# Performance work log

Hardware: AMD Instinct MI355X
Metric: run time of the kernel (lower is better)

## Reference

```python
import jax, jax.numpy as jnp
import numpy as np

B, L, D, H = 64, 1024, 64, 512
LN_EPS = 1e-5


def setup_inputs() -> dict:
    key = jax.random.key(0)
    ks = jax.random.split(key, 10)
    s = 1.0 / np.sqrt(H)  # torch GRU/Linear default uniform init bound
    u = lambda k, shape: jax.random.uniform(k, shape, jnp.float32, -s, s)
    return {
        "x": jax.random.normal(ks[0], (B, L, D), jnp.float32),
        "h0": jnp.zeros((1, B, H), jnp.float32),
        "W_ih": u(ks[1], (3 * H, D)),   # gate order: r, z, n
        "W_hh": u(ks[2], (3 * H, H)),
        "b_ih": u(ks[3], (3 * H,)),
        "b_hh": u(ks[4], (3 * H,)),
        "gamma": jnp.ones((H,), jnp.float32),
        "beta": jnp.zeros((H,), jnp.float32),
        "W_pred": u(ks[5], (D, H)),
        "b_pred": u(ks[6], (D,)),
    }


def _gru_forward(x, h0, W_ih, W_hh, b_ih, b_hh):
    # Precompute input projections for all timesteps in one big GEMM.
    gi = jnp.einsum('bld,gd->blg', x, W_ih) + b_ih          # (B, L, 3H)
    gi = jnp.moveaxis(gi, 1, 0)                              # (L, B, 3H)

    def step(h, gi_t):
        gh = h @ W_hh.T + b_hh                               # (B, 3H)
        i_r, i_z, i_n = jnp.split(gi_t, 3, axis=-1)
        h_r, h_z, h_n = jnp.split(gh, 3, axis=-1)
        r = jax.nn.sigmoid(i_r + h_r)
        z = jax.nn.sigmoid(i_z + h_z)
        n = jnp.tanh(i_n + r * h_n)
        h_new = (1.0 - z) * n + z * h                        # PyTorch GRU update
        return h_new, h_new

    hN, hs = jax.lax.scan(step, h0[0], gi)                   # hs: (L, B, H)
    return jnp.moveaxis(hs, 0, 1), hN[None]                  # (B, L, H), (1, B, H)


def reference(x, h0, W_ih, W_hh, b_ih, b_hh, gamma, beta, W_pred, b_pred):
    h_raw, hN = _gru_forward(x, h0, W_ih, W_hh, b_ih, b_hh)
    mu = h_raw.mean(-1, keepdims=True)
    var = ((h_raw - mu) ** 2).mean(-1, keepdims=True)
    h_seq = (h_raw - mu) * jax.lax.rsqrt(var + LN_EPS) * gamma + beta
    x_hat = h_seq @ W_pred.T + b_pred                        # (B, L, D)
    return h_seq, hN, x_hat
```

## Files before the change

### kernel.cpp

```cpp
#include <hip/hip_runtime.h>

typedef unsigned short ushort_t;
typedef unsigned int uint32;
typedef unsigned long long uint64;
typedef __attribute__((ext_vector_type(8))) __bf16 bf16x8;
typedef __attribute__((ext_vector_type(4))) float f32x4;

#define BB 64
#define LL 1024
#define DD 64
#define HH 512
#define HSEQ_N (BB * LL * HH)
#define HN_OFF HSEQ_N
#define XH_OFF (HSEQ_N + BB * HH)

#define NGRP 4
#define NBLK 8
#define NT 4
#define WS_HEX_OFF 1024
#define WS_PS_OFF (1024 + 2 * NGRP * 16 * 512 * 2)

__device__ __forceinline__ ushort_t f2bf(float f) {
  union { float f; uint32 i; } v; v.f = f;
  uint32 r = (v.i + 0x7fffu + ((v.i >> 16) & 1u)) >> 16;
  return (ushort_t)r;
}
__device__ __forceinline__ __bf16 u2b(ushort_t u) {
  union { ushort_t u; __bf16 b; } v; v.u = u; return v.b;
}
__device__ __forceinline__ bf16x8 cvt8(const float* p) {
  float4 a = *(const float4*)p;
  float4 b = *(const float4*)(p + 4);
  bf16x8 r;
  r[0] = u2b(f2bf(a.x)); r[1] = u2b(f2bf(a.y)); r[2] = u2b(f2bf(a.z)); r[3] = u2b(f2bf(a.w));
  r[4] = u2b(f2bf(b.x)); r[5] = u2b(f2bf(b.y)); r[6] = u2b(f2bf(b.z)); r[7] = u2b(f2bf(b.w));
  return r;
}
__device__ __forceinline__ float sigm(float x) { return 1.0f / (1.0f + __expf(-x)); }
__device__ __forceinline__ float tanh_f(float x) {
  x = fminf(20.f, fmaxf(-20.f, x));
  float e = __expf(2.0f * x);
  return (e - 1.0f) / (e + 1.0f);
}

__device__ __forceinline__ void st_u32_agent(uint32* p, uint32 v) {
  __hip_atomic_store(p, v, __ATOMIC_RELAXED, __HIP_MEMORY_SCOPE_AGENT);
}
__device__ __forceinline__ void st_u64_agent(uint64* p, uint64 v) {
  __hip_atomic_store(p, v, __ATOMIC_RELAXED, __HIP_MEMORY_SCOPE_AGENT);
}
__device__ __forceinline__ uint64 ld_u64_agent(const uint64* p) {
  return __hip_atomic_load((uint64*)p, __ATOMIC_RELAXED, __HIP_MEMORY_SCOPE_AGENT);
}

__global__ __launch_bounds__(768) void gru_kernel(
    const float* __restrict__ x, const float* __restrict__ h0,
    const float* __restrict__ Wih, const float* __restrict__ Whh,
    const float* __restrict__ bih, const float* __restrict__ bhh,
    const float* __restrict__ gamma, const float* __restrict__ beta,
    float* __restrict__ out, uint32* __restrict__ cnt,
    ushort_t* __restrict__ h_ex, float2* __restrict__ ps_ex)
{
  __shared__ __align__(16) ushort_t Abuf[16 * 520];
  __shared__ __align__(16) ushort_t xbuf[16 * 80];
  __shared__ float grz[8][16 * 17];
  __shared__ float2 statb[16];

  const int tid = threadIdx.x;
  const int v = tid >> 6, lane = tid & 63, lo = lane & 15, hi = lane >> 4;
  const int s = v >> 2, T = v & 3;
  const int g = blockIdx.x & 3, c = blockIdx.x >> 2;
  const int b0 = g * 16;
  const int colj = c * 64 + T * 16 + lo;
  const int rowW = s * HH + colj;

  bf16x8 wB[16], wI[2];
  {
    const float* wr = Whh + (size_t)rowW * HH + hi * 8;
    #pragma unroll
    for (int ks = 0; ks < 16; ++ks) wB[ks] = cvt8(wr + ks * 32);
    const float* wir = Wih + (size_t)rowW * DD + hi * 8;
    #pragma unroll
    for (int ks = 0; ks < 2; ++ks) wI[ks] = cvt8(wir + ks * 32);
  }
  const float bsum = bih[rowW] + bhh[rowW];
  const float bgh = bhh[rowW];
  const float bgi = bih[rowW];

  float hprev[4], gmv = 0.f, btv = 0.f;
  if (s == 2) {
    gmv = gamma[colj]; btv = beta[colj];
    #pragma unroll
    for (int i = 0; i < 4; ++i) hprev[i] = h0[(size_t)(b0 + hi * 4 + i) * HH + colj];
  }

  for (int i = tid; i < 16 * 512; i += 768) {
    int row = i >> 9, col = i & 511;
    Abuf[row * 520 + col] = f2bf(h0[(size_t)(b0 + row) * HH + col]);
  }
  for (int i = tid; i < 1024; i += 768) {
    int row = i >> 6, d = i & 63;
    xbuf[row * 80 + d] = f2bf(x[((size_t)(b0 + row) * LL + 0) * DD + d]);
  }
  __syncthreads();

  uint32* fb = cnt + g * 64;

  for (int t = 0; t < LL; ++t) {
    float xr[2];
    if (v > 0) {
      int t1 = (t + 1 < LL) ? (t + 1) : (LL - 1);
      int n = 0;
      for (int i = tid - 64; i < 1024; i += 704, ++n)
        xr[n] = x[((size_t)(b0 + (i >> 6)) * LL + t1) * DD + (i & 63)];
    }

    f32x4 a0, a1, agi;
    #pragma unroll
    for (int i = 0; i < 4; ++i) {
      a0[i] = (s < 2) ? bsum : bgh;
      a1[i] = 0.f;
      agi[i] = bgi;
    }
    #pragma unroll
    for (int ks = 0; ks < 2; ++ks) {
      bf16x8 av = *(const bf16x8*)&xbuf[lo * 80 + ks * 32 + hi * 8];
      if (s < 2) a0 = __builtin_amdgcn_mfma_f32_16x16x32_bf16(av, wI[ks], a0, 0, 0, 0);
      else       agi = __builtin_amdgcn_mfma_f32_16x16x32_bf16(av, wI[ks], agi, 0, 0, 0);
    }
    #pragma unroll
    for (int ks = 0; ks < 16; ++ks) {
      bf16x8 av = *(const bf16x8*)&Abuf[lo * 520 + ks * 32 + hi * 8];
      if (ks & 1) a1 = __builtin_amdgcn_mfma_f32_16x16x32_bf16(av, wB[ks], a1, 0, 0, 0);
      else        a0 = __builtin_amdgcn_mfma_f32_16x16x32_bf16(av, wB[ks], a0, 0, 0, 0);
    }
    f32x4 gacc;
    #pragma unroll
    for (int i = 0; i < 4; ++i) gacc[i] = a0[i] + a1[i];

    if (s < 2) {
      #pragma unroll
      for (int i = 0; i < 4; ++i) grz[s * 4 + T][(hi * 4 + i) * 17 + lo] = sigm(gacc[i]);
    }
    __syncthreads();

    if (s == 2) {
      float hn[4];
      #pragma unroll
      for (int i = 0; i < 4; ++i) {
        float r = grz[T][(hi * 4 + i) * 17 + lo];
        float z = grz[4 + T][(hi * 4 + i) * 17 + lo];
        float n = tanh_f(agi[i] + r * gacc[i]);
        hn[i] = z * (hprev[i] - n) + n;
      }
      uint32* hx32 = (uint32*)(h_ex + (size_t)(((t & 1) * NGRP + g) * 16) * 512);
      {
        uint32 pk[4];
        #pragma unroll
        for (int i = 0; i < 4; ++i) {
          uint32 m = (uint32)f2bf(hn[i]);
          uint32 o = (uint32)__shfl_xor((int)m, 1, 64);
          pk[i] = (lo & 1) ? ((o & 0xffffu) | (m << 16)) : (m | (o << 16));
        }
        int p = lo & 1;
        int cb = c * 32 + T * 8 + (lo >> 1);
        st_u32_agent(&hx32[(hi * 4 + 2 * p) * 256 + cb], pk[2 * p]);
        st_u32_agent(&hx32[(hi * 4 + 2 * p + 1) * 256 + cb], pk[2 * p + 1]);
      }
      #pragma unroll
      for (int i = 0; i < 4; ++i) {
        float sv = hn[i], sq = hn[i] * hn[i];
        #pragma unroll
        for (int m = 1; m < 16; m <<= 1) {
          sv += __shfl_xor(sv, m, 64);
          sq += __shfl_xor(sq, m, 64);
        }
        if (lo == 0) {
          float2* pp = ps_ex + ((size_t)((t & 1) * NGRP + g) * 32 + (c * 4 + T)) * 16;
          union { float2 f; uint64 u; } uu; uu.f = make_float2(sv, sq);
          st_u64_agent((uint64*)&pp[hi * 4 + i], uu.u);
        }
      }
      if (t == LL - 1) {
        #pragma unroll
        for (int i = 0; i < 4; ++i)
          out[(size_t)HN_OFF + (size_t)(b0 + hi * 4 + i) * HH + colj] = hn[i];
      }
      #pragma unroll
      for (int i = 0; i < 4; ++i) hprev[i] = hn[i];
    }
    __syncthreads();

    if (tid == 0) st_u32_agent(&fb[c * 8], (uint32)(t + 1));
    if (v > 0) {
      int n = 0;
      for (int i = tid - 64; i < 1024; i += 704, ++n)
        xbuf[(i >> 6) * 80 + (i & 63)] = f2bf(xr[n]);
    }
    if (v == 0) {
      const uint32 tgt = (uint32)(t + 1);
      while (true) {
        uint32 f = (lane < 8)
          ? __hip_atomic_load(&fb[lane * 8], __ATOMIC_RELAXED, __HIP_MEMORY_SCOPE_AGENT)
          : tgt;
        if (__all((int)(f >= tgt))) break;
        __builtin_amdgcn_s_sleep(1);
      }
    }
    __syncthreads();

    if (v != 3) {
      const uint64* hx8 = (const uint64*)(h_ex + (size_t)(((t & 1) * NGRP + g) * 16) * 512);
      int sid = (v < 3) ? tid : tid - 64;
      for (int i = sid; i < 2048; i += 704) {
        uint64 vv = ld_u64_agent(hx8 + i);
        int row = i >> 7, c8 = i & 127;
        *(uint64*)&Abuf[row * 520 + c8 * 4] = vv;
      }
    } else {
      int r = lane >> 2, q = lane & 3;
      const float2* pp = ps_ex + (size_t)((t & 1) * NGRP + g) * 32 * 16;
      float sv = 0.f, sq = 0.f;
      #pragma unroll
      for (int j = 0; j < 8; ++j) {
        int u = q * 8 + j;
        union { uint64 u64; float2 f; } uu;
        uu.u64 = ld_u64_agent((const uint64*)&pp[u * 16 + r]);
        sv += uu.f.x; sq += uu.f.y;
      }
      sv += __shfl_xor(sv, 1, 64); sq += __shfl_xor(sq, 1, 64);
      sv += __shfl_xor(sv, 2, 64); sq += __shfl_xor(sq, 2, 64);
      if (q == 0) {
        float mu = sv * (1.0f / 512.0f);
        float var = sq * (1.0f / 512.0f) - mu * mu;
        statb[r] = make_float2(mu, rsqrtf(var + 1e-5f));
      }
    }
    __syncthreads();

    if (s == 2) {
      #pragma unroll
      for (int i = 0; i < 4; ++i) {
        float2 st = statb[hi * 4 + i];
        float y = (hprev[i] - st.x) * st.y * gmv + btv;
        out[((size_t)(b0 + hi * 4 + i) * LL + t) * HH + colj] = y;
      }
    }
  }
}

__global__ __launch_bounds__(256) void pred_kernel(
    float* __restrict__ out, const float* __restrict__ Wp, const float* __restrict__ bp)
{
  const int tid = threadIdx.x;
  const int v = tid >> 6, lane = tid & 63, lo = lane & 15, hi = lane >> 4;
  const int d = v * 16 + lo;

  bf16x8 wP[16];
  const float* wr = Wp + (size_t)d * HH + hi * 8;
  #pragma unroll
  for (int ks = 0; ks < 16; ++ks) wP[ks] = cvt8(wr + ks * 32);
  const float bpf = bp[d];

  #pragma unroll
  for (int rt = 0; rt < 2; ++rt) {
    const size_t row0 = ((size_t)blockIdx.x * 2 + rt) * 16;
    const float* ap = out + (row0 + lo) * HH + hi * 8;
    f32x4 acc;
    #pragma unroll
    for (int i = 0; i < 4; ++i) acc[i] = 0.f;
    #pragma unroll
    for (int ks = 0; ks < 16; ++ks) {
      bf16x8 av = cvt8(ap + ks * 32);
      acc = __builtin_amdgcn_mfma_f32_16x16x32_bf16(av, wP[ks], acc, 0, 0, 0);
    }
    #pragma unroll
    for (int i = 0; i < 4; ++i)
      out[(size_t)XH_OFF + (row0 + hi * 4 + i) * DD + d] = acc[i] + bpf;
  }
}

extern "C" void kernel_launch(void* const* d_in, const int* in_sizes, int n_in,
                              void* d_out, int out_size, void* d_ws, size_t ws_size,
                              hipStream_t stream) {
  const float* x   = (const float*)d_in[0];
  const float* h0  = (const float*)d_in[1];
  const float* Wih = (const float*)d_in[2];
  const float* Whh = (const float*)d_in[3];
  const float* bih = (const float*)d_in[4];
  const float* bhh = (const float*)d_in[5];
  const float* gam = (const float*)d_in[6];
  const float* bet = (const float*)d_in[7];
  const float* Wp  = (const float*)d_in[8];
  const float* bp  = (const float*)d_in[9];
  float* out = (float*)d_out;

  uint32* cnt    = (uint32*)d_ws;
  ushort_t* h_ex = (ushort_t*)((char*)d_ws + WS_HEX_OFF);
  float2* ps_ex  = (float2*)((char*)d_ws + WS_PS_OFF);

  hipMemsetAsync(d_ws, 0, 1024, stream);

  hipLaunchKernelGGL(gru_kernel, dim3(NGRP * NBLK), dim3(768), 0, stream,
                     x, h0, Wih, Whh, bih, bhh, gam, bet, out, cnt, h_ex, ps_ex);
  hipLaunchKernelGGL(pred_kernel, dim3(BB * LL / 32), dim3(256), 0, stream,
                     out, Wp, bp);
}
```

Before: 4.836 ms.

## Replace flag barrier with per-word tagged exchange polling in GRU recurrence

The per-step cross-block synchronization (counter flags plus a polling wave and two block barriers) is replaced by tagging every exchanged hidden-state word and LayerNorm partial sum with the timestep. Readers spin directly on the data until every tag matches. This removes the flag round trip and one __syncthreads per step. The r/z waves now poll and fill Abuf while the n-gate waves compute, and x prefetch and the stats reduction move onto the n-gate waves. The cost is doubled exchange traffic, since each 32-bit payload now travels with a 32-bit tag, plus a larger workspace memset.

```diff
diff --git a/kernel.cpp b/kernel.cpp
--- a/kernel.cpp
+++ b/kernel.cpp
@@ -16,9 +16,9 @@
 
 #define NGRP 4
 #define NBLK 8
-#define NT 4
 #define WS_HEX_OFF 1024
-#define WS_PS_OFF (1024 + 2 * NGRP * 16 * 512 * 2)
+#define WS_PS_OFF (1024 + 2 * NGRP * 16 * 256 * 8)
+#define WS_TOTAL (WS_PS_OFF + 2 * NGRP * 32 * 16 * 2 * 8)
 
 __device__ __forceinline__ ushort_t f2bf(float f) {
   union { float f; uint32 i; } v; v.f = f;
@@ -43,9 +43,6 @@
   return (e - 1.0f) / (e + 1.0f);
 }
 
-__device__ __forceinline__ void st_u32_agent(uint32* p, uint32 v) {
-  __hip_atomic_store(p, v, __ATOMIC_RELAXED, __HIP_MEMORY_SCOPE_AGENT);
-}
 __device__ __forceinline__ void st_u64_agent(uint64* p, uint64 v) {
   __hip_atomic_store(p, v, __ATOMIC_RELAXED, __HIP_MEMORY_SCOPE_AGENT);
 }
@@ -58,8 +55,7 @@
     const float* __restrict__ Wih, const float* __restrict__ Whh,
     const float* __restrict__ bih, const float* __restrict__ bhh,
     const float* __restrict__ gamma, const float* __restrict__ beta,
-    float* __restrict__ out, uint32* __restrict__ cnt,
-    ushort_t* __restrict__ h_ex, float2* __restrict__ ps_ex)
+    float* __restrict__ out, uint64* __restrict__ h_ex, uint64* __restrict__ ps_ex)
 {
   __shared__ __align__(16) ushort_t Abuf[16 * 520];
   __shared__ __align__(16) ushort_t xbuf[16 * 80];
@@ -104,15 +100,16 @@
   }
   __syncthreads();
 
-  uint32* fb = cnt + g * 64;
-
   for (int t = 0; t < LL; ++t) {
-    float xr[2];
-    if (v > 0) {
+    float xr[6];
+    if (v >= 9) {
       int t1 = (t + 1 < LL) ? (t + 1) : (LL - 1);
-      int n = 0;
-      for (int i = tid - 64; i < 1024; i += 704, ++n)
-        xr[n] = x[((size_t)(b0 + (i >> 6)) * LL + t1) * DD + (i & 63)];
+      int sid = tid - 576;
+      #pragma unroll
+      for (int k = 0; k < 6; ++k) {
+        int i = sid + k * 192;
+        if (i < 1024) xr[k] = x[((size_t)(b0 + (i >> 6)) * LL + t1) * DD + (i & 63)];
+      }
     }
 
     f32x4 a0, a1, agi;
@@ -144,7 +141,29 @@
     }
     __syncthreads();
 
-    if (s == 2) {
+    const uint32 tag = (uint32)(t + 1);
+    uint64* hx = h_ex + (size_t)((t & 1) * NGRP + g) * 4096;
+
+    if (s < 2) {
+      uint64 vals[8];
+      #pragma unroll
+      for (int k = 0; k < 8; ++k) vals[k] = ld_u64_agent(hx + tid + k * 512);
+      while (true) {
+        int bad = 0;
+        #pragma unroll
+        for (int k = 0; k < 8; ++k) bad |= ((uint32)vals[k] != tag);
+        if (!bad) break;
+        #pragma unroll
+        for (int k = 0; k < 8; ++k)
+          if ((uint32)vals[k] != tag) vals[k] = ld_u64_agent(hx + tid + k * 512);
+      }
+      #pragma unroll
+      for (int k = 0; k < 8; ++k) {
+        int idx = tid + k * 512;
+        int row = idx >> 8, cb = idx & 255;
+        *(uint32*)&Abuf[row * 520 + cb * 2] = (uint32)(vals[k] >> 32);
+      }
+    } else {
       float hn[4];
       #pragma unroll
       for (int i = 0; i < 4; ++i) {
@@ -153,7 +172,6 @@
         float n = tanh_f(agi[i] + r * gacc[i]);
         hn[i] = z * (hprev[i] - n) + n;
       }
-      uint32* hx32 = (uint32*)(h_ex + (size_t)(((t & 1) * NGRP + g) * 16) * 512);
       {
         uint32 pk[4];
         #pragma unroll
@@ -164,9 +182,11 @@
         }
         int p = lo & 1;
         int cb = c * 32 + T * 8 + (lo >> 1);
-        st_u32_agent(&hx32[(hi * 4 + 2 * p) * 256 + cb], pk[2 * p]);
-        st_u32_agent(&hx32[(hi * 4 + 2 * p + 1) * 256 + cb], pk[2 * p + 1]);
-      }
+        int r0 = hi * 4 + 2 * p;
+        st_u64_agent(&hx[r0 * 256 + cb], ((uint64)pk[2 * p] << 32) | tag);
+        st_u64_agent(&hx[(r0 + 1) * 256 + cb], ((uint64)pk[2 * p + 1] << 32) | tag);
+      }
+      uint64* pu = ps_ex + (size_t)((t & 1) * NGRP + g) * 1024;
       #pragma unroll
       for (int i = 0; i < 4; ++i) {
         float sv = hn[i], sq = hn[i] * hn[i];
@@ -176,9 +196,10 @@
           sq += __shfl_xor(sq, m, 64);
         }
         if (lo == 0) {
-          float2* pp = ps_ex + ((size_t)((t & 1) * NGRP + g) * 32 + (c * 4 + T)) * 16;
-          union { float2 f; uint64 u; } uu; uu.f = make_float2(sv, sq);
-          st_u64_agent((uint64*)&pp[hi * 4 + i], uu.u);
+          union { float f; uint32 u; } fv, fq; fv.f = sv; fq.f = sq;
+          int e = ((c * 4 + T) * 16 + (hi * 4 + i)) * 2;
+          st_u64_agent(&pu[e], ((uint64)fv.u << 32) | tag);
+          st_u64_agent(&pu[e + 1], ((uint64)fq.u << 32) | tag);
         }
       }
       if (t == LL - 1) {
@@ -188,52 +209,54 @@
       }
       #pragma unroll
       for (int i = 0; i < 4; ++i) hprev[i] = hn[i];
-    }
-    __syncthreads();
-
-    if (tid == 0) st_u32_agent(&fb[c * 8], (uint32)(t + 1));
-    if (v > 0) {
-      int n = 0;
-      for (int i = tid - 64; i < 1024; i += 704, ++n)
-        xbuf[(i >> 6) * 80 + (i & 63)] = f2bf(xr[n]);
-    }
-    if (v == 0) {
-      const uint32 tgt = (uint32)(t + 1);
-      while (true) {
-        uint32 f = (lane < 8)
-          ? __hip_atomic_load(&fb[lane * 8], __ATOMIC_RELAXED, __HIP_MEMORY_SCOPE_AGENT)
-          : tgt;
-        if (__all((int)(f >= tgt))) break;
-        __builtin_amdgcn_s_sleep(1);
-      }
-    }
-    __syncthreads();
-
-    if (v != 3) {
-      const uint64* hx8 = (const uint64*)(h_ex + (size_t)(((t & 1) * NGRP + g) * 16) * 512);
-      int sid = (v < 3) ? tid : tid - 64;
-      for (int i = sid; i < 2048; i += 704) {
-        uint64 vv = ld_u64_agent(hx8 + i);
-        int row = i >> 7, c8 = i & 127;
-        *(uint64*)&Abuf[row * 520 + c8 * 4] = vv;
-      }
-    } else {
-      int r = lane >> 2, q = lane & 3;
-      const float2* pp = ps_ex + (size_t)((t & 1) * NGRP + g) * 32 * 16;
-      float sv = 0.f, sq = 0.f;
-      #pragma unroll
-      for (int j = 0; j < 8; ++j) {
-        int u = q * 8 + j;
-        union { uint64 u64; float2 f; } uu;
-        uu.u64 = ld_u64_agent((const uint64*)&pp[u * 16 + r]);
-        sv += uu.f.x; sq += uu.f.y;
-      }
-      sv += __shfl_xor(sv, 1, 64); sq += __shfl_xor(sq, 1, 64);
-      sv += __shfl_xor(sv, 2, 64); sq += __shfl_xor(sq, 2, 64);
-      if (q == 0) {
-        float mu = sv * (1.0f / 512.0f);
-        float var = sq * (1.0f / 512.0f) - mu * mu;
-        statb[r] = make_float2(mu, rsqrtf(var + 1e-5f));
+
+      if (v >= 9) {
+        int sid = tid - 576;
+        #pragma unroll
+        for (int k = 0; k < 6; ++k) {
+          int i = sid + k * 192;
+          if (i < 1024) xbuf[(i >> 6) * 80 + (i & 63)] = f2bf(xr[k]);
+        }
+      }
+      if (v == 8) {
+        int r = lane >> 2, q = lane & 3;
+        const uint64* pb = ps_ex + (size_t)((t & 1) * NGRP + g) * 1024;
+        uint64 va[8], vb[8];
+        #pragma unroll
+        for (int j = 0; j < 8; ++j) {
+          int u = q * 8 + j;
+          int e = (u * 16 + r) * 2;
+          va[j] = ld_u64_agent(pb + e);
+          vb[j] = ld_u64_agent(pb + e + 1);
+        }
+        while (true) {
+          int bad = 0;
+          #pragma unroll
+          for (int j = 0; j < 8; ++j)
+            bad |= ((uint32)va[j] != tag) | ((uint32)vb[j] != tag);
+          if (!bad) break;
+          #pragma unroll
+          for (int j = 0; j < 8; ++j) {
+            int u = q * 8 + j;
+            int e = (u * 16 + r) * 2;
+            if ((uint32)va[j] != tag) va[j] = ld_u64_agent(pb + e);
+            if ((uint32)vb[j] != tag) vb[j] = ld_u64_agent(pb + e + 1);
+          }
+        }
+        float sv = 0.f, sq = 0.f;
+        #pragma unroll
+        for (int j = 0; j < 8; ++j) {
+          union { uint32 u; float f; } ua, ub;
+          ua.u = (uint32)(va[j] >> 32); ub.u = (uint32)(vb[j] >> 32);
+          sv += ua.f; sq += ub.f;
+        }
+        sv += __shfl_xor(sv, 1, 64); sq += __shfl_xor(sq, 1, 64);
+        sv += __shfl_xor(sv, 2, 64); sq += __shfl_xor(sq, 2, 64);
+        if (q == 0) {
+          float mu = sv * (1.0f / 512.0f);
+          float var = sq * (1.0f / 512.0f) - mu * mu;
+          statb[r] = make_float2(mu, rsqrtf(var + 1e-5f));
+        }
       }
     }
     __syncthreads();
@@ -295,14 +318,13 @@
   const float* bp  = (const float*)d_in[9];
   float* out = (float*)d_out;
 
-  uint32* cnt    = (uint32*)d_ws;
-  ushort_t* h_ex = (ushort_t*)((char*)d_ws + WS_HEX_OFF);
-  float2* ps_ex  = (float2*)((char*)d_ws + WS_PS_OFF);
-
-  hipMemsetAsync(d_ws, 0, 1024, stream);
+  uint64* h_ex = (uint64*)((char*)d_ws + WS_HEX_OFF);
+  uint64* ps_ex = (uint64*)((char*)d_ws + WS_PS_OFF);
+
+  hipMemsetAsync(d_ws, 0, WS_TOTAL, stream);
 
   hipLaunchKernelGGL(gru_kernel, dim3(NGRP * NBLK), dim3(768), 0, stream,
-                     x, h0, Wih, Whh, bih, bhh, gam, bet, out, cnt, h_ex, ps_ex);
+                     x, h0, Wih, Whh, bih, bhh, gam, bet, out, h_ex, ps_ex);
   hipLaunchKernelGGL(pred_kernel, dim3(BB * LL / 32), dim3(256), 0, stream,
                      out, Wp, bp);
 }
```

New measurement: 6.575 ms. +35.9%, slower.

## Use per-wave flags and 4-deep exchange buffers to remove per-step block barriers

Applied to the files above, without the earlier changes.

Each n-gate wave now publishes its own readiness flag after draining its global stores, instead of one thread per block signalling after a block-wide barrier. Non-n waves spin on all 32 flags and pull the exchanged hidden state directly. One n-gate wave computes the LayerNorm statistics while the others stage the next x slice. The exchange buffers are quadruple-buffered so fewer block syncs are needed per timestep, which aims to shorten the serial critical path of the recurrence. In exchange there is more flag-polling traffic and subtler ordering requirements between waves.

```diff
diff --git a/kernel.cpp b/kernel.cpp
--- a/kernel.cpp
+++ b/kernel.cpp
@@ -16,9 +16,9 @@
 
 #define NGRP 4
 #define NBLK 8
-#define NT 4
 #define WS_HEX_OFF 1024
-#define WS_PS_OFF (1024 + 2 * NGRP * 16 * 512 * 2)
+#define WS_PS_OFF (1024 + 4 * NGRP * 4096 * 4)
+#define WS_FLAG_BYTES 1024
 
 __device__ __forceinline__ ushort_t f2bf(float f) {
   union { float f; uint32 i; } v; v.f = f;
@@ -49,6 +49,9 @@
 __device__ __forceinline__ void st_u64_agent(uint64* p, uint64 v) {
   __hip_atomic_store(p, v, __ATOMIC_RELAXED, __HIP_MEMORY_SCOPE_AGENT);
 }
+__device__ __forceinline__ uint32 ld_u32_agent(const uint32* p) {
+  return __hip_atomic_load((uint32*)p, __ATOMIC_RELAXED, __HIP_MEMORY_SCOPE_AGENT);
+}
 __device__ __forceinline__ uint64 ld_u64_agent(const uint64* p) {
   return __hip_atomic_load((uint64*)p, __ATOMIC_RELAXED, __HIP_MEMORY_SCOPE_AGENT);
 }
@@ -59,7 +62,7 @@
     const float* __restrict__ bih, const float* __restrict__ bhh,
     const float* __restrict__ gamma, const float* __restrict__ beta,
     float* __restrict__ out, uint32* __restrict__ cnt,
-    ushort_t* __restrict__ h_ex, float2* __restrict__ ps_ex)
+    uint32* __restrict__ h_ex, float2* __restrict__ ps_ex)
 {
   __shared__ __align__(16) ushort_t Abuf[16 * 520];
   __shared__ __align__(16) ushort_t xbuf[16 * 80];
@@ -107,12 +110,15 @@
   uint32* fb = cnt + g * 64;
 
   for (int t = 0; t < LL; ++t) {
-    float xr[2];
-    if (v > 0) {
+    float xr[6];
+    if (v >= 9) {
       int t1 = (t + 1 < LL) ? (t + 1) : (LL - 1);
-      int n = 0;
-      for (int i = tid - 64; i < 1024; i += 704, ++n)
-        xr[n] = x[((size_t)(b0 + (i >> 6)) * LL + t1) * DD + (i & 63)];
+      int sid = tid - 576;
+      #pragma unroll
+      for (int k = 0; k < 6; ++k) {
+        int i = sid + k * 192;
+        if (i < 1024) xr[k] = x[((size_t)(b0 + (i >> 6)) * LL + t1) * DD + (i & 63)];
+      }
     }
 
     f32x4 a0, a1, agi;
@@ -143,6 +149,9 @@
       for (int i = 0; i < 4; ++i) grz[s * 4 + T][(hi * 4 + i) * 17 + lo] = sigm(gacc[i]);
     }
     __syncthreads();
+
+    const uint32 tag = (uint32)(t + 1);
+    const int par = t & 3;
 
     if (s == 2) {
       float hn[4];
@@ -153,7 +162,7 @@
         float n = tanh_f(agi[i] + r * gacc[i]);
         hn[i] = z * (hprev[i] - n) + n;
       }
-      uint32* hx32 = (uint32*)(h_ex + (size_t)(((t & 1) * NGRP + g) * 16) * 512);
+      uint32* hx32 = h_ex + (size_t)(par * NGRP + g) * 4096;
       {
         uint32 pk[4];
         #pragma unroll
@@ -164,9 +173,11 @@
         }
         int p = lo & 1;
         int cb = c * 32 + T * 8 + (lo >> 1);
-        st_u32_agent(&hx32[(hi * 4 + 2 * p) * 256 + cb], pk[2 * p]);
-        st_u32_agent(&hx32[(hi * 4 + 2 * p + 1) * 256 + cb], pk[2 * p + 1]);
-      }
+        int r0 = hi * 4 + 2 * p;
+        st_u32_agent(&hx32[r0 * 256 + cb], pk[2 * p]);
+        st_u32_agent(&hx32[(r0 + 1) * 256 + cb], pk[2 * p + 1]);
+      }
+      float2* pp = ps_ex + (size_t)(par * NGRP + g) * 512 + (c * 4 + T) * 16;
       #pragma unroll
       for (int i = 0; i < 4; ++i) {
         float sv = hn[i], sq = hn[i] * hn[i];
@@ -176,7 +187,6 @@
           sq += __shfl_xor(sq, m, 64);
         }
         if (lo == 0) {
-          float2* pp = ps_ex + ((size_t)((t & 1) * NGRP + g) * 32 + (c * 4 + T)) * 16;
           union { float2 f; uint64 u; } uu; uu.f = make_float2(sv, sq);
           st_u64_agent((uint64*)&pp[hi * 4 + i], uu.u);
         }
@@ -188,52 +198,56 @@
       }
       #pragma unroll
       for (int i = 0; i < 4; ++i) hprev[i] = hn[i];
-    }
-    __syncthreads();
-
-    if (tid == 0) st_u32_agent(&fb[c * 8], (uint32)(t + 1));
-    if (v > 0) {
-      int n = 0;
-      for (int i = tid - 64; i < 1024; i += 704, ++n)
-        xbuf[(i >> 6) * 80 + (i & 63)] = f2bf(xr[n]);
-    }
-    if (v == 0) {
-      const uint32 tgt = (uint32)(t + 1);
+
+      asm volatile("s_waitcnt vmcnt(0)" ::: "memory");
+      __builtin_amdgcn_sched_barrier(0);
+      if (lane == 0) st_u32_agent(&fb[c * 4 + T], tag);
+
+      if (v >= 9) {
+        int sid = tid - 576;
+        #pragma unroll
+        for (int k = 0; k < 6; ++k) {
+          int i = sid + k * 192;
+          if (i < 1024) xbuf[(i >> 6) * 80 + (i & 63)] = f2bf(xr[k]);
+        }
+      }
+      if (v == 8) {
+        while (true) {
+          uint32 f = (lane < 32) ? ld_u32_agent(&fb[lane]) : tag;
+          if (__all((int)(f >= tag))) break;
+          __builtin_amdgcn_s_sleep(1);
+        }
+        int r = lane >> 2, q = lane & 3;
+        const uint64* pb = (const uint64*)(ps_ex + (size_t)(par * NGRP + g) * 512);
+        float sv = 0.f, sq = 0.f;
+        #pragma unroll
+        for (int j = 0; j < 8; ++j) {
+          int u = q * 8 + j;
+          union { uint64 u64; float2 f; } uu;
+          uu.u64 = ld_u64_agent(pb + u * 16 + r);
+          sv += uu.f.x; sq += uu.f.y;
+        }
+        sv += __shfl_xor(sv, 1, 64); sq += __shfl_xor(sq, 1, 64);
+        sv += __shfl_xor(sv, 2, 64); sq += __shfl_xor(sq, 2, 64);
+        if (q == 0) {
+          float mu = sv * (1.0f / 512.0f);
+          float var = sq * (1.0f / 512.0f) - mu * mu;
+          statb[r] = make_float2(mu, rsqrtf(var + 1e-5f));
+        }
+      }
+    } else if (t + 1 < LL) {
       while (true) {
-        uint32 f = (lane < 8)
-          ? __hip_atomic_load(&fb[lane * 8], __ATOMIC_RELAXED, __HIP_MEMORY_SCOPE_AGENT)
-          : tgt;
-        if (__all((int)(f >= tgt))) break;
+        uint32 f = (lane < 32) ? ld_u32_agent(&fb[lane]) : tag;
+        if (__all((int)(f >= tag))) break;
         __builtin_amdgcn_s_sleep(1);
       }
-    }
-    __syncthreads();
-
-    if (v != 3) {
-      const uint64* hx8 = (const uint64*)(h_ex + (size_t)(((t & 1) * NGRP + g) * 16) * 512);
-      int sid = (v < 3) ? tid : tid - 64;
-      for (int i = sid; i < 2048; i += 704) {
-        uint64 vv = ld_u64_agent(hx8 + i);
-        int row = i >> 7, c8 = i & 127;
+      const uint64* hx8 = (const uint64*)(h_ex + (size_t)(par * NGRP + g) * 4096);
+      #pragma unroll
+      for (int k = 0; k < 4; ++k) {
+        int idx = v * 256 + k * 64 + lane;
+        uint64 vv = ld_u64_agent(hx8 + idx);
+        int row = idx >> 7, c8 = idx & 127;
         *(uint64*)&Abuf[row * 520 + c8 * 4] = vv;
-      }
-    } else {
-      int r = lane >> 2, q = lane & 3;
-      const float2* pp = ps_ex + (size_t)((t & 1) * NGRP + g) * 32 * 16;
-      float sv = 0.f, sq = 0.f;
-      #pragma unroll
-      for (int j = 0; j < 8; ++j) {
-        int u = q * 8 + j;
-        union { uint64 u64; float2 f; } uu;
-        uu.u64 = ld_u64_agent((const uint64*)&pp[u * 16 + r]);
-        sv += uu.f.x; sq += uu.f.y;
-      }
-      sv += __shfl_xor(sv, 1, 64); sq += __shfl_xor(sq, 1, 64);
-      sv += __shfl_xor(sv, 2, 64); sq += __shfl_xor(sq, 2, 64);
-      if (q == 0) {
-        float mu = sv * (1.0f / 512.0f);
-        float var = sq * (1.0f / 512.0f) - mu * mu;
-        statb[r] = make_float2(mu, rsqrtf(var + 1e-5f));
       }
     }
     __syncthreads();
@@ -295,11 +309,11 @@
   const float* bp  = (const float*)d_in[9];
   float* out = (float*)d_out;
 
-  uint32* cnt    = (uint32*)d_ws;
-  ushort_t* h_ex = (ushort_t*)((char*)d_ws + WS_HEX_OFF);
-  float2* ps_ex  = (float2*)((char*)d_ws + WS_PS_OFF);
-
-  hipMemsetAsync(d_ws, 0, 1024, stream);
+  uint32* cnt   = (uint32*)d_ws;
+  uint32* h_ex  = (uint32*)((char*)d_ws + WS_HEX_OFF);
+  float2* ps_ex = (float2*)((char*)d_ws + WS_PS_OFF);
+
+  hipMemsetAsync(d_ws, 0, WS_FLAG_BYTES, stream);
 
   hipLaunchKernelGGL(gru_kernel, dim3(NGRP * NBLK), dim3(768), 0, stream,
                      x, h0, Wih, Whh, bih, bhh, gam, bet, out, cnt, h_ex, ps_ex);
```

Result: slower. 5.852 ms (+21.0%).
